# Performance work log

Hardware: AMD Instinct MI355X
Metric: run time of the kernel (lower is better)

The kernel has to match this reference:

```python
import jax, jax.numpy as jnp
import numpy as np

B, T, C = 2, 2048, 1024
H = 16
HD = C // H  # head_dim = 64


def setup_inputs() -> dict:
    key = jax.random.key(0)
    ks = jax.random.split(key, 5)
    s = 0.02
    return {
        "x": jax.random.normal(ks[0], (B, T, C), dtype=jnp.float32),
        "Wqkv": jax.random.normal(ks[1], (C, 3 * C), dtype=jnp.float32) * s,
        "bqkv": jax.random.normal(ks[2], (3 * C,), dtype=jnp.float32) * s,
        "Wproj": jax.random.normal(ks[3], (C, C), dtype=jnp.float32) * s,
        "bproj": jax.random.normal(ks[4], (C,), dtype=jnp.float32) * s,
    }


def reference(x, Wqkv, bqkv, Wproj, bproj):
    b, t, c = x.shape
    qkv = x @ Wqkv + bqkv  # [B,T,3C]
    q, k, v = jnp.split(qkv, 3, axis=-1)
    # [B,T,C] -> [B,H,T,HD]
    q = q.reshape(b, t, H, HD).transpose(0, 2, 1, 3)
    k = k.reshape(b, t, H, HD).transpose(0, 2, 1, 3)
    v = v.reshape(b, t, H, HD).transpose(0, 2, 1, 3)
    scale = 1.0 / jnp.sqrt(jnp.float32(HD))
    att = jnp.einsum('bhqd,bhkd->bhqk', q, k) * scale  # [B,H,T,T]
    causal = jnp.tril(jnp.ones((t, t), dtype=bool))
    att = jnp.where(causal[None, None], att, jnp.float32(-jnp.inf))
    att = jax.nn.softmax(att, axis=-1)
    y = jnp.einsum('bhqk,bhkd->bhqd', att, v)  # [B,H,T,HD]
    y = y.transpose(0, 2, 1, 3).reshape(b, t, c)
    return y @ Wproj + bproj
```

## Files before the change

kernel.cpp:

```cpp
#include <hip/hip_runtime.h>

typedef unsigned short u16;
typedef __attribute__((ext_vector_type(4))) float f32x4;
typedef __attribute__((ext_vector_type(8))) short short8;

#define AS1 __attribute__((address_space(1)))
#define AS3 __attribute__((address_space(3)))

#define B_  2
#define T_  2048
#define C_  1024
#define H_  16
#define HD_ 64
#define N3C 3072
#define BT_ 4096

__device__ __forceinline__ u16 f2bf(float x) {
    unsigned u = __float_as_uint(x);
    u += 0x7fff + ((u >> 16) & 1);
    return (u16)(u >> 16);
}

__global__ __launch_bounds__(256)
void conv_all(const float* __restrict__ x, u16* __restrict__ xb,
              const float* __restrict__ Wq, u16* __restrict__ WqT,
              const float* __restrict__ Wp, u16* __restrict__ WpT) {
    __shared__ float tile[64][68];
    const int tid = threadIdx.x;
    const int b = blockIdx.x;
    if (b < 4096) {
        int i = b * 256 + tid;
        float4 f = ((const float4*)x)[i];
        ushort4 o;
        o.x = f2bf(f.x); o.y = f2bf(f.y); o.z = f2bf(f.z); o.w = f2bf(f.w);
        ((ushort4*)xb)[i] = o;
        return;
    }
    const float* W; u16* WT; int N, k0, n0;
    if (b < 4096 + 768) {
        int bb = b - 4096; W = Wq; WT = WqT; N = N3C;
        n0 = (bb % 48) * 64; k0 = (bb / 48) * 64;
    } else {
        int bb = b - 4864; W = Wp; WT = WpT; N = C_;
        n0 = (bb % 16) * 64; k0 = (bb / 16) * 64;
    }
    #pragma unroll
    for (int i = 0; i < 4; ++i) {
        int slot = tid + i * 256;
        int row = slot >> 4, c4 = (slot & 15) * 4;
        *(float4*)&tile[row][c4] = *(const float4*)&W[(size_t)(k0 + row) * N + n0 + c4];
    }
    __syncthreads();
    #pragma unroll
    for (int i = 0; i < 4; ++i) {
        int slot = tid + i * 256;
        int nn = slot >> 4, k4 = (slot & 15) * 4;
        ushort4 o;
        o.x = f2bf(tile[k4 + 0][nn]); o.y = f2bf(tile[k4 + 1][nn]);
        o.z = f2bf(tile[k4 + 2][nn]); o.w = f2bf(tile[k4 + 3][nn]);
        *(ushort4*)&WT[(size_t)(n0 + nn) * 1024 + k0 + k4] = o;
    }
}

__device__ __forceinline__ void gemm_core(const u16* __restrict__ A, const u16* __restrict__ BT,
                                          u16* As, u16* Bs, int m0, int n0,
                                          f32x4 (&acc)[4][4]) {
    const int tid = threadIdx.x;
    const int lane = tid & 63, w = tid >> 6;
    const int l15 = lane & 15, quad = lane >> 4;
    const int row0 = (w >> 1) * 64, col0 = (w & 1) * 64;
    const int srow = lane >> 3;
    const int schunk = (lane & 7) ^ srow;

    for (int k0 = 0; k0 < 1024; k0 += 64) {
        __syncthreads();
        #pragma unroll
        for (int j = 0; j < 4; ++j) {
            int rbase = w * 32 + j * 8;
            const u16* ga = A  + (size_t)(m0 + rbase + srow) * 1024 + k0 + schunk * 8;
            const u16* gb = BT + (size_t)(n0 + rbase + srow) * 1024 + k0 + schunk * 8;
            __builtin_amdgcn_global_load_lds((const AS1 void*)ga, (AS3 void*)(As + rbase * 64), 16, 0, 0);
            __builtin_amdgcn_global_load_lds((const AS1 void*)gb, (AS3 void*)(Bs + rbase * 64), 16, 0, 0);
        }
        __syncthreads();
        #pragma unroll
        for (int s = 0; s < 2; ++s) {
            short8 a[4], b[4];
            #pragma unroll
            for (int rt = 0; rt < 4; ++rt) {
                int row = row0 + rt * 16 + l15;
                a[rt] = *(const short8*)&As[row * 64 + (((s * 4 + quad) ^ (l15 & 7)) * 8)];
            }
            #pragma unroll
            for (int ct = 0; ct < 4; ++ct) {
                int row = col0 + ct * 16 + l15;
                b[ct] = *(const short8*)&Bs[row * 64 + (((s * 4 + quad) ^ (l15 & 7)) * 8)];
            }
            #pragma unroll
            for (int rt = 0; rt < 4; ++rt)
                #pragma unroll
                for (int ct = 0; ct < 4; ++ct)
                    acc[rt][ct] = __builtin_amdgcn_mfma_f32_16x16x32_bf16(a[rt], b[ct], acc[rt][ct], 0, 0, 0);
        }
    }
}

__global__ __launch_bounds__(256)
void qkv_gemm(const u16* __restrict__ A, const u16* __restrict__ BT,
              const float* __restrict__ bias,
              u16* __restrict__ q, u16* __restrict__ k, u16* __restrict__ vT) {
    __shared__ __align__(16) u16 As[128 * 64];
    __shared__ __align__(16) u16 Bs[128 * 64];
    const int m0 = blockIdx.y * 128, n0 = blockIdx.x * 128;
    f32x4 acc[4][4] = {};
    gemm_core(A, BT, As, Bs, m0, n0, acc);

    const int tid = threadIdx.x;
    const int lane = tid & 63, w = tid >> 6;
    const int l15 = lane & 15, quad = lane >> 4;
    const int row0 = (w >> 1) * 64, col0 = (w & 1) * 64;
    const int which = n0 >> 10;

    #pragma unroll
    for (int ct = 0; ct < 4; ++ct) {
        int n = n0 + col0 + ct * 16 + l15;
        int nl = n & 1023, h = nl >> 6, d = nl & 63;
        float bv = bias[n];
        #pragma unroll
        for (int rt = 0; rt < 4; ++rt) {
            int mb = m0 + row0 + rt * 16 + quad * 4;
            int bb = mb >> 11, t0 = mb & 2047;
            f32x4 v4 = acc[rt][ct];
            if (which == 0) {
                size_t base = ((size_t)(bb * H_ + h) * T_ + t0) * HD_ + d;
                #pragma unroll
                for (int r = 0; r < 4; ++r)
                    q[base + (size_t)r * HD_] = f2bf((v4[r] + bv) * 0.125f);
            } else if (which == 1) {
                size_t base = ((size_t)(bb * H_ + h) * T_ + t0) * HD_ + d;
                #pragma unroll
                for (int r = 0; r < 4; ++r)
                    k[base + (size_t)r * HD_] = f2bf(v4[r] + bv);
            } else {
                ushort4 o;
                o.x = f2bf(v4[0] + bv); o.y = f2bf(v4[1] + bv);
                o.z = f2bf(v4[2] + bv); o.w = f2bf(v4[3] + bv);
                *(ushort4*)&vT[((size_t)(bb * H_ + h) * HD_ + d) * T_ + t0] = o;
            }
        }
    }
}

__global__ __launch_bounds__(256)
void attn(const u16* __restrict__ q, const u16* __restrict__ k,
          const u16* __restrict__ vT, u16* __restrict__ y) {
    __shared__ __align__(16) u16 Ks[64 * 64];
    __shared__ __align__(16) u16 Vs[64 * 64];
    __shared__ __align__(16) u16 Ps[4 * 16 * 72];
    const int tid = threadIdx.x;
    const int lane = tid & 63, w = tid >> 6;
    const int l15 = lane & 15, quad = lane >> 4;
    const int srow = lane >> 3, schunk = (lane & 7) ^ srow;
    const int idx = blockIdx.x;
    const int bh = idx & 31;
    const int p = idx >> 5;
    const int qtH = 31 - p, qtL = p;
    const u16* qp = q  + (size_t)bh * T_ * HD_;
    const u16* kp = k  + (size_t)bh * T_ * HD_;
    const u16* vp = vT + (size_t)bh * HD_ * T_;
    u16* Pw = Ps + w * 16 * 72;

    const int qrowH = qtH * 64 + w * 16 + l15;
    const int qrowL = qtL * 64 + w * 16 + l15;
    short8 qfH[2], qfL[2];
    #pragma unroll
    for (int s = 0; s < 2; ++s) {
        qfH[s] = *(const short8*)&qp[(size_t)qrowH * HD_ + s * 32 + quad * 8];
        qfL[s] = *(const short8*)&qp[(size_t)qrowL * HD_ + s * 32 + quad * 8];
    }

    f32x4 oH[4] = {}, oL[4] = {};
    float lH = 0.f, lL = 0.f;

    for (int kt = 0; kt <= qtH; ++kt) {
        const int kb = kt * 64;
        __syncthreads();
        #pragma unroll
        for (int j = 0; j < 2; ++j) {
            int row = w * 16 + j * 8 + srow;
            __builtin_amdgcn_global_load_lds(
                (const AS1 void*)(kp + (size_t)(kb + row) * HD_ + schunk * 8),
                (AS3 void*)(Ks + (w * 16 + j * 8) * 64), 16, 0, 0);
            __builtin_amdgcn_global_load_lds(
                (const AS1 void*)(vp + (size_t)row * T_ + kb + schunk * 8),
                (AS3 void*)(Vs + (w * 16 + j * 8) * 64), 16, 0, 0);
        }
        __syncthreads();

        short8 ka[4][2], va[4][2];
        #pragma unroll
        for (int ct = 0; ct < 4; ++ct)
            #pragma unroll
            for (int s = 0; s < 2; ++s) {
                int xo = ((s * 4 + quad) ^ (l15 & 7)) * 8;
                ka[ct][s] = *(const short8*)&Ks[(ct * 16 + l15) * 64 + xo];
                va[ct][s] = *(const short8*)&Vs[(ct * 16 + l15) * 64 + xo];
            }

        {
            f32x4 st[4] = {};
            #pragma unroll
            for (int s = 0; s < 2; ++s)
                #pragma unroll
                for (int ct = 0; ct < 4; ++ct)
                    st[ct] = __builtin_amdgcn_mfma_f32_16x16x32_bf16(ka[ct][s], qfH[s], st[ct], 0, 0, 0);
            const bool last = (kt == qtH);
            float psum = 0.f;
            #pragma unroll
            for (int ct = 0; ct < 4; ++ct) {
                float pe[4];
                #pragma unroll
                for (int r = 0; r < 4; ++r) {
                    pe[r] = __expf(st[ct][r]);
                    if (last && (kb + ct * 16 + quad * 4 + r) > qrowH) pe[r] = 0.f;
                    psum += pe[r];
                }
                uint2 pk;
                pk.x = (unsigned)f2bf(pe[0]) | ((unsigned)f2bf(pe[1]) << 16);
                pk.y = (unsigned)f2bf(pe[2]) | ((unsigned)f2bf(pe[3]) << 16);
                *(uint2*)&Pw[l15 * 72 + ct * 16 + quad * 4] = pk;
            }
            lH += psum;
            asm volatile("s_waitcnt lgkmcnt(0)" ::: "memory");
            #pragma unroll
            for (int s = 0; s < 2; ++s) {
                short8 pb = *(const short8*)&Pw[l15 * 72 + s * 32 + quad * 8];
                #pragma unroll
                for (int n = 0; n < 4; ++n)
                    oH[n] = __builtin_amdgcn_mfma_f32_16x16x32_bf16(va[n][s], pb, oH[n], 0, 0, 0);
            }
        }
        if (kt <= qtL) {
            f32x4 st[4] = {};
            #pragma unroll
            for (int s = 0; s < 2; ++s)
                #pragma unroll
                for (int ct = 0; ct < 4; ++ct)
                    st[ct] = __builtin_amdgcn_mfma_f32_16x16x32_bf16(ka[ct][s], qfL[s], st[ct], 0, 0, 0);
            const bool last = (kt == qtL);
            float psum = 0.f;
            #pragma unroll
            for (int ct = 0; ct < 4; ++ct) {
                float pe[4];
                #pragma unroll
                for (int r = 0; r < 4; ++r) {
                    pe[r] = __expf(st[ct][r]);
                    if (last && (kb + ct * 16 + quad * 4 + r) > qrowL) pe[r] = 0.f;
                    psum += pe[r];
                }
                uint2 pk;
                pk.x = (unsigned)f2bf(pe[0]) | ((unsigned)f2bf(pe[1]) << 16);
                pk.y = (unsigned)f2bf(pe[2]) | ((unsigned)f2bf(pe[3]) << 16);
                *(uint2*)&Pw[l15 * 72 + ct * 16 + quad * 4] = pk;
            }
            lL += psum;
            asm volatile("s_waitcnt lgkmcnt(0)" ::: "memory");
            #pragma unroll
            for (int s = 0; s < 2; ++s) {
                short8 pb = *(const short8*)&Pw[l15 * 72 + s * 32 + quad * 8];
                #pragma unroll
                for (int n = 0; n < 4; ++n)
                    oL[n] = __builtin_amdgcn_mfma_f32_16x16x32_bf16(va[n][s], pb, oL[n], 0, 0, 0);
            }
        }
    }

    lH += __shfl_xor(lH, 16); lH += __shfl_xor(lH, 32);
    lL += __shfl_xor(lL, 16); lL += __shfl_xor(lL, 32);
    const float invH = 1.f / lH, invL = 1.f / lL;
    const int bb = bh >> 4, h = bh & 15;
    #pragma unroll
    for (int n = 0; n < 4; ++n) {
        uint2 pk;
        pk.x = (unsigned)f2bf(oH[n][0] * invH) | ((unsigned)f2bf(oH[n][1] * invH) << 16);
        pk.y = (unsigned)f2bf(oH[n][2] * invH) | ((unsigned)f2bf(oH[n][3] * invH) << 16);
        *(uint2*)&y[((size_t)(bb * T_ + qrowH)) * C_ + h * 64 + n * 16 + quad * 4] = pk;
        uint2 pl;
        pl.x = (unsigned)f2bf(oL[n][0] * invL) | ((unsigned)f2bf(oL[n][1] * invL) << 16);
        pl.y = (unsigned)f2bf(oL[n][2] * invL) | ((unsigned)f2bf(oL[n][3] * invL) << 16);
        *(uint2*)&y[((size_t)(bb * T_ + qrowL)) * C_ + h * 64 + n * 16 + quad * 4] = pl;
    }
}

__global__ __launch_bounds__(256)
void proj_gemm(const u16* __restrict__ A, const u16* __restrict__ BT,
               const float* __restrict__ bias, float* __restrict__ out) {
    __shared__ __align__(16) u16 As[128 * 64];
    __shared__ __align__(16) u16 Bs[128 * 64];
    const int m0 = blockIdx.y * 128, n0 = blockIdx.x * 128;
    f32x4 acc[4][4] = {};
    gemm_core(A, BT, As, Bs, m0, n0, acc);

    const int tid = threadIdx.x;
    const int lane = tid & 63, w = tid >> 6;
    const int l15 = lane & 15, quad = lane >> 4;
    const int row0 = (w >> 1) * 64, col0 = (w & 1) * 64;

    #pragma unroll
    for (int ct = 0; ct < 4; ++ct) {
        int n = n0 + col0 + ct * 16 + l15;
        float bv = bias[n];
        #pragma unroll
        for (int rt = 0; rt < 4; ++rt) {
            int mb = m0 + row0 + rt * 16 + quad * 4;
            f32x4 v4 = acc[rt][ct];
            #pragma unroll
            for (int r = 0; r < 4; ++r)
                out[(size_t)(mb + r) * 1024 + n] = v4[r] + bv;
        }
    }
}

extern "C" void kernel_launch(void* const* d_in, const int* in_sizes, int n_in,
                              void* d_out, int out_size, void* d_ws, size_t ws_size,
                              hipStream_t stream) {
    const float* x     = (const float*)d_in[0];
    const float* Wqkv  = (const float*)d_in[1];
    const float* bqkv  = (const float*)d_in[2];
    const float* Wproj = (const float*)d_in[3];
    const float* bproj = (const float*)d_in[4];

    u16* xb     = (u16*)d_ws;
    u16* WqkvT  = xb + (size_t)4 * 1024 * 1024;
    u16* WprojT = WqkvT + (size_t)3 * 1024 * 1024;
    u16* q      = WprojT + (size_t)1024 * 1024;
    u16* kk     = q + (size_t)4 * 1024 * 1024;
    u16* vT     = kk + (size_t)4 * 1024 * 1024;
    u16* y      = vT + (size_t)4 * 1024 * 1024;

    conv_all<<<5120, 256, 0, stream>>>(x, xb, Wqkv, WqkvT, Wproj, WprojT);
    qkv_gemm<<<dim3(N3C / 128, BT_ / 128), 256, 0, stream>>>(xb, WqkvT, bqkv, q, kk, vT);
    attn<<<512, 256, 0, stream>>>(q, kk, vT, y);
    proj_gemm<<<dim3(C_ / 128, BT_ / 128), 256, 0, stream>>>(y, WprojT, bproj, (float*)d_out);
}
```

Baseline: 192.7 us.

## Double-buffer LDS tiles in GEMM and attention to overlap loads with MFMA

Adds a second LDS buffer to the shared GEMM core and to the attention kernel's K/V tiles. The next tile is prefetched with global_load_lds while the current one is consumed, using explicit vmcnt waits and barriers in place of the two __syncthreads per iteration. The goal is to hide global-memory latency behind the MFMA work. In exchange, LDS use doubles (64KB per GEMM block), which can lower occupancy, and correctness now relies on the hand-counted vmcnt values.

```diff
diff --git a/kernel.cpp b/kernel.cpp
--- a/kernel.cpp
+++ b/kernel.cpp
@@ -63,8 +63,8 @@
 }
 
 __device__ __forceinline__ void gemm_core(const u16* __restrict__ A, const u16* __restrict__ BT,
-                                          u16* As, u16* Bs, int m0, int n0,
-                                          f32x4 (&acc)[4][4]) {
+                                          u16* As, u16* Bs,
+                                          int m0, int n0, f32x4 (&acc)[4][4]) {
     const int tid = threadIdx.x;
     const int lane = tid & 63, w = tid >> 6;
     const int l15 = lane & 15, quad = lane >> 4;
@@ -72,29 +72,43 @@
     const int srow = lane >> 3;
     const int schunk = (lane & 7) ^ srow;
 
-    for (int k0 = 0; k0 < 1024; k0 += 64) {
-        __syncthreads();
+    auto stage = [&](int buf, int k0) {
         #pragma unroll
         for (int j = 0; j < 4; ++j) {
             int rbase = w * 32 + j * 8;
             const u16* ga = A  + (size_t)(m0 + rbase + srow) * 1024 + k0 + schunk * 8;
             const u16* gb = BT + (size_t)(n0 + rbase + srow) * 1024 + k0 + schunk * 8;
-            __builtin_amdgcn_global_load_lds((const AS1 void*)ga, (AS3 void*)(As + rbase * 64), 16, 0, 0);
-            __builtin_amdgcn_global_load_lds((const AS1 void*)gb, (AS3 void*)(Bs + rbase * 64), 16, 0, 0);
-        }
-        __syncthreads();
+            __builtin_amdgcn_global_load_lds((const AS1 void*)ga,
+                (AS3 void*)(As + buf * (128 * 64) + rbase * 64), 16, 0, 0);
+            __builtin_amdgcn_global_load_lds((const AS1 void*)gb,
+                (AS3 void*)(Bs + buf * (128 * 64) + rbase * 64), 16, 0, 0);
+        }
+    };
+
+    stage(0, 0);
+    #pragma unroll
+    for (int it = 0; it < 16; ++it) {
+        const int cur = it & 1;
+        if (it + 1 < 16) {
+            stage(cur ^ 1, (it + 1) * 64);
+            asm volatile("s_waitcnt vmcnt(8)\n\ts_barrier" ::: "memory");
+        } else {
+            asm volatile("s_waitcnt vmcnt(0)\n\ts_barrier" ::: "memory");
+        }
+        const u16* Ac = As + cur * (128 * 64);
+        const u16* Bc = Bs + cur * (128 * 64);
         #pragma unroll
         for (int s = 0; s < 2; ++s) {
             short8 a[4], b[4];
             #pragma unroll
             for (int rt = 0; rt < 4; ++rt) {
                 int row = row0 + rt * 16 + l15;
-                a[rt] = *(const short8*)&As[row * 64 + (((s * 4 + quad) ^ (l15 & 7)) * 8)];
+                a[rt] = *(const short8*)&Ac[row * 64 + (((s * 4 + quad) ^ (l15 & 7)) * 8)];
             }
             #pragma unroll
             for (int ct = 0; ct < 4; ++ct) {
                 int row = col0 + ct * 16 + l15;
-                b[ct] = *(const short8*)&Bs[row * 64 + (((s * 4 + quad) ^ (l15 & 7)) * 8)];
+                b[ct] = *(const short8*)&Bc[row * 64 + (((s * 4 + quad) ^ (l15 & 7)) * 8)];
             }
             #pragma unroll
             for (int rt = 0; rt < 4; ++rt)
@@ -102,6 +116,7 @@
                 for (int ct = 0; ct < 4; ++ct)
                     acc[rt][ct] = __builtin_amdgcn_mfma_f32_16x16x32_bf16(a[rt], b[ct], acc[rt][ct], 0, 0, 0);
         }
+        asm volatile("s_waitcnt lgkmcnt(0)\n\ts_barrier" ::: "memory");
     }
 }
 
@@ -109,8 +124,8 @@
 void qkv_gemm(const u16* __restrict__ A, const u16* __restrict__ BT,
               const float* __restrict__ bias,
               u16* __restrict__ q, u16* __restrict__ k, u16* __restrict__ vT) {
-    __shared__ __align__(16) u16 As[128 * 64];
-    __shared__ __align__(16) u16 Bs[128 * 64];
+    __shared__ __align__(16) u16 As[2 * 128 * 64];
+    __shared__ __align__(16) u16 Bs[2 * 128 * 64];
     const int m0 = blockIdx.y * 128, n0 = blockIdx.x * 128;
     f32x4 acc[4][4] = {};
     gemm_core(A, BT, As, Bs, m0, n0, acc);
@@ -154,8 +169,8 @@
 __global__ __launch_bounds__(256)
 void attn(const u16* __restrict__ q, const u16* __restrict__ k,
           const u16* __restrict__ vT, u16* __restrict__ y) {
-    __shared__ __align__(16) u16 Ks[64 * 64];
-    __shared__ __align__(16) u16 Vs[64 * 64];
+    __shared__ __align__(16) u16 Ks[2 * 64 * 64];
+    __shared__ __align__(16) u16 Vs[2 * 64 * 64];
     __shared__ __align__(16) u16 Ps[4 * 16 * 72];
     const int tid = threadIdx.x;
     const int lane = tid & 63, w = tid >> 6;
@@ -179,23 +194,35 @@
         qfL[s] = *(const short8*)&qp[(size_t)qrowL * HD_ + s * 32 + quad * 8];
     }
 
-    f32x4 oH[4] = {}, oL[4] = {};
-    float lH = 0.f, lL = 0.f;
-
-    for (int kt = 0; kt <= qtH; ++kt) {
+    auto stage = [&](int buf, int kt) {
         const int kb = kt * 64;
-        __syncthreads();
         #pragma unroll
         for (int j = 0; j < 2; ++j) {
             int row = w * 16 + j * 8 + srow;
             __builtin_amdgcn_global_load_lds(
                 (const AS1 void*)(kp + (size_t)(kb + row) * HD_ + schunk * 8),
-                (AS3 void*)(Ks + (w * 16 + j * 8) * 64), 16, 0, 0);
+                (AS3 void*)(Ks + buf * (64 * 64) + (w * 16 + j * 8) * 64), 16, 0, 0);
             __builtin_amdgcn_global_load_lds(
                 (const AS1 void*)(vp + (size_t)row * T_ + kb + schunk * 8),
-                (AS3 void*)(Vs + (w * 16 + j * 8) * 64), 16, 0, 0);
-        }
-        __syncthreads();
+                (AS3 void*)(Vs + buf * (64 * 64) + (w * 16 + j * 8) * 64), 16, 0, 0);
+        }
+    };
+
+    f32x4 oH[4] = {}, oL[4] = {};
+    float lH = 0.f, lL = 0.f;
+    stage(0, 0);
+
+    for (int kt = 0; kt <= qtH; ++kt) {
+        const int kb = kt * 64;
+        const int cur = kt & 1;
+        if (kt < qtH) {
+            stage(cur ^ 1, kt + 1);
+            asm volatile("s_waitcnt vmcnt(4)\n\ts_barrier" ::: "memory");
+        } else {
+            asm volatile("s_waitcnt vmcnt(0)\n\ts_barrier" ::: "memory");
+        }
+        const u16* Kc = Ks + cur * (64 * 64);
+        const u16* Vc = Vs + cur * (64 * 64);
 
         short8 ka[4][2], va[4][2];
         #pragma unroll
@@ -203,8 +230,8 @@
             #pragma unroll
             for (int s = 0; s < 2; ++s) {
                 int xo = ((s * 4 + quad) ^ (l15 & 7)) * 8;
-                ka[ct][s] = *(const short8*)&Ks[(ct * 16 + l15) * 64 + xo];
-                va[ct][s] = *(const short8*)&Vs[(ct * 16 + l15) * 64 + xo];
+                ka[ct][s] = *(const short8*)&Kc[(ct * 16 + l15) * 64 + xo];
+                va[ct][s] = *(const short8*)&Vc[(ct * 16 + l15) * 64 + xo];
             }
 
         {
@@ -273,6 +300,7 @@
                     oL[n] = __builtin_amdgcn_mfma_f32_16x16x32_bf16(va[n][s], pb, oL[n], 0, 0, 0);
             }
         }
+        asm volatile("s_waitcnt lgkmcnt(0)\n\ts_barrier" ::: "memory");
     }
 
     lH += __shfl_xor(lH, 16); lH += __shfl_xor(lH, 32);
@@ -295,8 +323,8 @@
 __global__ __launch_bounds__(256)
 void proj_gemm(const u16* __restrict__ A, const u16* __restrict__ BT,
                const float* __restrict__ bias, float* __restrict__ out) {
-    __shared__ __align__(16) u16 As[128 * 64];
-    __shared__ __align__(16) u16 Bs[128 * 64];
+    __shared__ __align__(16) u16 As[2 * 128 * 64];
+    __shared__ __align__(16) u16 Bs[2 * 128 * 64];
     const int m0 = blockIdx.y * 128, n0 = blockIdx.x * 128;
     f32x4 acc[4][4] = {};
     gemm_core(A, BT, As, Bs, m0, n0, acc);
```

Measured after the change: 184.5 us. 4.2% less time.
